# Kernel tuning notes

Hardware: AMD Instinct MI355X
Metric: run time of the kernel (lower is better)

Reference implementation:

```python
import jax, jax.numpy as jnp
import numpy as np

LAMBDA = 10.0
BETA = 10.0
W = 5  # window size per axis (5,5,5); padding=2 hardcoded in original
DN = ('NCDHW', 'OIDHW', 'NCDHW')


def box_mean(x):
    """Uniform 5x5x5 box-filter mean with zero padding=2, via separable 1D convs."""
    specs = [((1, 1, W, 1, 1), [(2, 2), (0, 0), (0, 0)]),
             ((1, 1, 1, W, 1), [(0, 0), (2, 2), (0, 0)]),
             ((1, 1, 1, 1, W), [(0, 0), (0, 0), (2, 2)])]
    for kshape, pads in specs:
        k = jnp.full(kshape, 1.0 / W, dtype=x.dtype)
        x = jax.lax.conv_general_dilated(x, k, (1, 1, 1), pads, dimension_numbers=DN)
    return x


def lcc_loss(gt, pred):
    omega = gt.size
    d_gt = gt - box_mean(gt)
    d_pred = pred - box_mean(pred)
    num = jnp.square(jnp.sum(d_gt * d_pred))
    den = jnp.sum(jnp.square(d_gt)) * jnp.sum(jnp.square(d_pred))
    den = jnp.maximum(den, 1e-5)
    return -(1.0 / omega) * (num / den)


def reg_field_loss(reg_gt, reg_pred):
    omega = reg_gt.size
    return jnp.sqrt(jnp.sum(jnp.square(reg_pred - reg_gt))) / omega


def tversky_loss2(seg_gt, seg_pred):
    den = jnp.maximum(jnp.sum(seg_gt + seg_pred), 1e-5)
    return -0.5 * jnp.sum(2.0 * seg_gt * seg_pred) / den


def setup_inputs() -> dict:
    key = jax.random.key(0)
    ks = jax.random.split(key, 10)
    shp_f = (2, 3, 128, 128, 128)
    shp_i = (2, 1, 128, 128, 128)
    return {
        'F_0': jax.random.normal(ks[0], shp_f, jnp.float32),
        'F_0g': jax.random.normal(ks[1], shp_f, jnp.float32),
        'I_0': jax.random.uniform(ks[2], shp_i, jnp.float32),
        'I_0R': jax.random.uniform(ks[3], shp_i, jnp.float32),
        'I_1': jax.random.uniform(ks[4], shp_i, jnp.float32),
        'I_1R': jax.random.uniform(ks[5], shp_i, jnp.float32),
        'S_0': jax.random.uniform(ks[6], shp_i, jnp.float32),
        'S_0g': jax.random.uniform(ks[7], shp_i, jnp.float32),
        'S_1': jax.random.uniform(ks[8], shp_i, jnp.float32),
        'S_1g': jax.random.uniform(ks[9], shp_i, jnp.float32),
    }


def reference(F_0, F_0g, I_0, I_0R, I_1, I_1R, S_0, S_0g, S_1, S_1g):
    return (reg_field_loss(F_0, F_0g)
            + LAMBDA * (lcc_loss(I_0, I_0R) + lcc_loss(I_1, I_1R))
            + BETA * (tversky_loss2(S_0, S_0g) + tversky_loss2(S_1, S_1g)))
```

## Files before the change

### kernel.cpp

```cpp
#include <hip/hip_runtime.h>
#include <math.h>

#define VOL   (128*128*128)
#define PLANE (128*128)

#define LCC_BLOCKS   1024
#define SQ_BLOCKS    1024
#define TV_BLOCKS    256
#define TOTAL_BLOCKS (LCC_BLOCKS + SQ_BLOCKS + 2 * TV_BLOCKS)


__device__ __forceinline__ double wave_reduce_d(double v) {
    #pragma unroll
    for (int off = 32; off > 0; off >>= 1)
        v += __shfl_down(v, off, 64);
    return v;
}

__device__ __forceinline__ void block_reduce1_atomic(double a, double* dst) {
    __shared__ double s1[4];
    int lane = threadIdx.x & 63;
    int wave = threadIdx.x >> 6;
    a = wave_reduce_d(a);
    if (lane == 0) s1[wave] = a;
    __syncthreads();
    if (threadIdx.x == 0) {
        double A = s1[0] + s1[1] + s1[2] + s1[3];
        atomicAdd(&dst[0], A);
    }
}

__device__ __forceinline__ void block_reduce2_atomic(double a, double b, double* dst) {
    __shared__ double s2[2][4];
    int lane = threadIdx.x & 63;
    int wave = threadIdx.x >> 6;
    a = wave_reduce_d(a);
    b = wave_reduce_d(b);
    if (lane == 0) { s2[0][wave] = a; s2[1][wave] = b; }
    __syncthreads();
    if (threadIdx.x == 0) {
        atomicAdd(&dst[0], s2[0][0] + s2[0][1] + s2[0][2] + s2[0][3]);
        atomicAdd(&dst[1], s2[1][0] + s2[1][1] + s2[1][2] + s2[1][3]);
    }
}

__device__ __forceinline__ void block_reduce3_atomic(double a, double b, double c, double* dst) {
    __shared__ double s3[3][4];
    int lane = threadIdx.x & 63;
    int wave = threadIdx.x >> 6;
    a = wave_reduce_d(a);
    b = wave_reduce_d(b);
    c = wave_reduce_d(c);
    if (lane == 0) { s3[0][wave] = a; s3[1][wave] = b; s3[2][wave] = c; }
    __syncthreads();
    if (threadIdx.x == 0) {
        atomicAdd(&dst[0], s3[0][0] + s3[0][1] + s3[0][2] + s3[0][3]);
        atomicAdd(&dst[1], s3[1][0] + s3[1][1] + s3[1][2] + s3[1][3]);
        atomicAdd(&dst[2], s3[2][0] + s3[2][1] + s3[2][2] + s3[2][3]);
    }
}


__global__ void zero_ws_kernel(double* ws) {
    if (threadIdx.x < 16) ws[threadIdx.x] = 0.0;
}


__global__ __launch_bounds__(256) void mega_kernel(
    const float* __restrict__ F0,  const float* __restrict__ F0g,
    const float* __restrict__ I0,  const float* __restrict__ I0R,
    const float* __restrict__ I1,  const float* __restrict__ I1R,
    const float* __restrict__ S0,  const float* __restrict__ S0g,
    const float* __restrict__ S1,  const float* __restrict__ S1g,
    double* __restrict__ ws)
{
    int b = blockIdx.x;
    int tid = threadIdx.x;

    if (b < LCC_BLOCKS) {
        __shared__ float ybuf[2 * 8 * 128];
        __shared__ float dbuf[8 * 128];

        int pair = b >> 9;
        int r  = b & 511;
        int y0 = (r & 15) << 3;
        int z0 = ((r >> 4) & 15) << 3;
        int n  = r >> 8;

        const float* gt = pair ? I1  : I0;
        const float* pr = pair ? I1R : I0R;
        double* dst = ws + (pair ? 4 : 1);

        int x = tid & 127;
        int g = tid >> 7;
        const float* V = (g ? pr : gt) + (size_t)n * VOL;

        float a1 = 0.f, a2 = 0.f, a3 = 0.f;
        float ps[5][8];
        float cent1[8], cent2[8];
        float v[12];

        float* yb = ybuf + g * 1024;

        {
            int zp = z0 - 2;
            bool zin = (zp >= 0);
            #pragma unroll
            for (int j = 0; j < 12; ++j) {
                int gy = y0 - 2 + j;
                v[j] = (zin && gy >= 0 && gy < 128)
                         ? V[(size_t)zp * PLANE + (size_t)gy * 128 + x] : 0.0f;
            }
        }

        #pragma unroll
        for (int it = 0; it < 12; ++it) {
            int zp = z0 - 2 + it;
            #pragma unroll
            for (int k = 0; k < 8; ++k)
                yb[k * 128 + x] = v[k] + v[k+1] + v[k+2] + v[k+3] + v[k+4];

            float vn[12];
            if (it < 11) {
                int zq = zp + 1;
                bool zin = (zq < 128);
                bool zlo = (zq >= 0);
                #pragma unroll
                for (int j = 0; j < 12; ++j) {
                    int gy = y0 - 2 + j;
                    vn[j] = (zin && zlo && gy >= 0 && gy < 128)
                              ? V[(size_t)zq * PLANE + (size_t)gy * 128 + x] : 0.0f;
                }
            }
            __syncthreads();

            #pragma unroll
            for (int k = 0; k < 8; ++k) {
                float s = yb[k * 128 + x];
                if (x >= 2)   s += yb[k * 128 + x - 2];
                if (x >= 1)   s += yb[k * 128 + x - 1];
                if (x <= 126) s += yb[k * 128 + x + 1];
                if (x <= 125) s += yb[k * 128 + x + 2];
                ps[it % 5][k] = s;
            }

            float d[8];
            if (it >= 4) {
                #pragma unroll
                for (int k = 0; k < 8; ++k) {
                    float m = (ps[0][k] + ps[1][k] + ps[2][k] + ps[3][k] + ps[4][k])
                              * (1.0f / 125.0f);
                    d[k] = cent2[k] - m;
                }
                if (g) {
                    #pragma unroll
                    for (int k = 0; k < 8; ++k) {
                        dbuf[k * 128 + x] = d[k];
                        a3 += d[k] * d[k];
                    }
                }
            }
            __syncthreads();
            if (it >= 4 && g == 0) {
                #pragma unroll
                for (int k = 0; k < 8; ++k) {
                    float dp = dbuf[k * 128 + x];
                    a1 += d[k] * dp;
                    a2 += d[k] * d[k];
                }
            }

            #pragma unroll
            for (int k = 0; k < 8; ++k) { cent2[k] = cent1[k]; cent1[k] = v[k + 2]; }
            if (it < 11) {
                #pragma unroll
                for (int j = 0; j < 12; ++j) v[j] = vn[j];
            }
        }
        block_reduce3_atomic((double)a1, (double)a2, (double)a3, dst);

    } else if (b < LCC_BLOCKS + SQ_BLOCKS) {
        int bid = b - LCC_BLOCKS;
        const float4* A = (const float4*)F0;
        const float4* B = (const float4*)F0g;
        int n4 = 12582912 / 4;
        int idx = bid * 256 + tid;
        int stride = SQ_BLOCKS * 256;
        float acc = 0.f;
        for (int i = idx; i < n4; i += stride) {
            float4 xx = A[i], yy = B[i];
            float d0 = yy.x - xx.x, d1 = yy.y - xx.y;
            float d2 = yy.z - xx.z, d3 = yy.w - xx.w;
            acc += (d0 * d0 + d1 * d1) + (d2 * d2 + d3 * d3);
        }
        block_reduce1_atomic((double)acc, &ws[0]);

    } else {
        int bid = b - (LCC_BLOCKS + SQ_BLOCKS);
        int pair = bid >= TV_BLOCKS;
        bid -= pair ? TV_BLOCKS : 0;
        const float4* Gp = (const float4*)(pair ? S1 : S0);
        const float4* Pp = (const float4*)(pair ? S1g : S0g);
        double* dst = ws + (pair ? 9 : 7);
        int n4 = 4194304 / 4;
        int idx = bid * 256 + tid;
        int stride = TV_BLOCKS * 256;
        float asum = 0.f, aprod = 0.f;
        for (int i = idx; i < n4; i += stride) {
            float4 xx = Gp[i], yy = Pp[i];
            asum  += (xx.x + yy.x) + (xx.y + yy.y) + (xx.z + yy.z) + (xx.w + yy.w);
            aprod += (xx.x * yy.x + xx.y * yy.y) + (xx.z * yy.z + xx.w * yy.w);
        }
        block_reduce2_atomic((double)asum, (double)aprod, dst);
    }
}

__global__ void finalize_kernel(const double* __restrict__ ws, float* out) {
    if (threadIdx.x == 0 && blockIdx.x == 0) {
        double reg = sqrt(ws[0]) / 12582912.0;

        double num0 = ws[1] * ws[1];
        double den0 = ws[2] * ws[3];
        if (den0 < 1e-5) den0 = 1e-5;
        double l0 = -(1.0 / 4194304.0) * (num0 / den0);

        double num1 = ws[4] * ws[4];
        double den1 = ws[5] * ws[6];
        if (den1 < 1e-5) den1 = 1e-5;
        double l1 = -(1.0 / 4194304.0) * (num1 / den1);

        double td0 = ws[7]; if (td0 < 1e-5) td0 = 1e-5;
        double t0 = -ws[8] / td0;
        double td1 = ws[9]; if (td1 < 1e-5) td1 = 1e-5;
        double t1 = -ws[10] / td1;

        out[0] = (float)(reg + 10.0 * (l0 + l1) + 10.0 * (t0 + t1));
    }
}


extern "C" void kernel_launch(void* const* d_in, const int* in_sizes, int n_in,
                              void* d_out, int out_size, void* d_ws, size_t ws_size,
                              hipStream_t stream) {
    double* ws = (double*)d_ws;
    float* out = (float*)d_out;

    const float* F0  = (const float*)d_in[0];
    const float* F0g = (const float*)d_in[1];
    const float* I0  = (const float*)d_in[2];
    const float* I0R = (const float*)d_in[3];
    const float* I1  = (const float*)d_in[4];
    const float* I1R = (const float*)d_in[5];
    const float* S0  = (const float*)d_in[6];
    const float* S0g = (const float*)d_in[7];
    const float* S1  = (const float*)d_in[8];
    const float* S1g = (const float*)d_in[9];

    zero_ws_kernel<<<1, 64, 0, stream>>>(ws);
    mega_kernel<<<TOTAL_BLOCKS, 256, 0, stream>>>(F0, F0g, I0, I0R, I1, I1R,
                                                  S0, S0g, S1, S1g, ws);
    finalize_kernel<<<1, 64, 0, stream>>>(ws, out);
}
```

Measured before the change: 260.6 us.

## Restructure LCC box filter into per-wave tiles and interleave block roles

```diff
diff --git a/kernel.cpp b/kernel.cpp
--- a/kernel.cpp
+++ b/kernel.cpp
@@ -4,10 +4,10 @@
 #define VOL   (128*128*128)
 #define PLANE (128*128)
 
-#define LCC_BLOCKS   1024
+#define LCC_BLOCKS   512
 #define SQ_BLOCKS    1024
-#define TV_BLOCKS    256
-#define TOTAL_BLOCKS (LCC_BLOCKS + SQ_BLOCKS + 2 * TV_BLOCKS)
+#define TV_BLOCKS    512
+#define TOTAL_BLOCKS 2048
 
 
 __device__ __forceinline__ double wave_reduce_d(double v) {
@@ -24,10 +24,8 @@
     a = wave_reduce_d(a);
     if (lane == 0) s1[wave] = a;
     __syncthreads();
-    if (threadIdx.x == 0) {
-        double A = s1[0] + s1[1] + s1[2] + s1[3];
-        atomicAdd(&dst[0], A);
-    }
+    if (threadIdx.x == 0)
+        atomicAdd(&dst[0], s1[0] + s1[1] + s1[2] + s1[3]);
 }
 
 __device__ __forceinline__ void block_reduce2_atomic(double a, double b, double* dst) {
@@ -76,118 +74,117 @@
 {
     int b = blockIdx.x;
     int tid = threadIdx.x;
-
-    if (b < LCC_BLOCKS) {
-        __shared__ float ybuf[2 * 8 * 128];
-        __shared__ float dbuf[8 * 128];
-
-        int pair = b >> 9;
-        int r  = b & 511;
-        int y0 = (r & 15) << 3;
-        int z0 = ((r >> 4) & 15) << 3;
-        int n  = r >> 8;
-
-        const float* gt = pair ? I1  : I0;
-        const float* pr = pair ? I1R : I0R;
+    int r = b & 3;
+
+    if (r == 0) {
+        __shared__ float xrow[4][2][4][68];
+
+        int lb = b >> 2;
+        int w  = tid >> 6;
+        int l  = tid & 63;
+        int wid = lb * 4 + w;
+        int pair  = wid >> 10;
+        int batch = (wid >> 9) & 1;
+        int zs    = (wid >> 6) & 7;
+        int yt    = (wid >> 1) & 31;
+        int xt    = wid & 1;
+        int x0 = xt << 6, y0 = yt << 2, z0 = zs << 4;
+
+        const float* Vg = (pair ? I1  : I0)  + (size_t)batch * VOL;
+        const float* Vp = (pair ? I1R : I0R) + (size_t)batch * VOL;
         double* dst = ws + (pair ? 4 : 1);
 
-        int x = tid & 127;
-        int g = tid >> 7;
-        const float* V = (g ? pr : gt) + (size_t)n * VOL;
-
+        int x  = x0 + l;
+        int hx = x0 + ((l < 2) ? (l - 2) : (62 + l));
+        int hxc = hx < 0 ? 0 : (hx > 127 ? 127 : hx);
+        bool hok = (hx >= 0) && (hx < 128);
+        int hslot = (l < 2) ? l : (64 + l);
+
+        float (*rowg)[68] = xrow[w][0];
+        float (*rowp)[68] = xrow[w][1];
+
+        float psg[5][4], psp[5][4];
+        float cg1[4] = {0,0,0,0}, cg2[4] = {0,0,0,0};
+        float cp1[4] = {0,0,0,0}, cp2[4] = {0,0,0,0};
         float a1 = 0.f, a2 = 0.f, a3 = 0.f;
-        float ps[5][8];
-        float cent1[8], cent2[8];
-        float v[12];
-
-        float* yb = ybuf + g * 1024;
-
-        {
-            int zp = z0 - 2;
-            bool zin = (zp >= 0);
+
+        for (int o = 0; o < 4; ++o) {
             #pragma unroll
-            for (int j = 0; j < 12; ++j) {
-                int gy = y0 - 2 + j;
-                v[j] = (zin && gy >= 0 && gy < 128)
-                         ? V[(size_t)zp * PLANE + (size_t)gy * 128 + x] : 0.0f;
-            }
-        }
-
-        #pragma unroll
-        for (int it = 0; it < 12; ++it) {
-            int zp = z0 - 2 + it;
-            #pragma unroll
-            for (int k = 0; k < 8; ++k)
-                yb[k * 128 + x] = v[k] + v[k+1] + v[k+2] + v[k+3] + v[k+4];
-
-            float vn[12];
-            if (it < 11) {
-                int zq = zp + 1;
-                bool zin = (zq < 128);
-                bool zlo = (zq >= 0);
-                #pragma unroll
-                for (int j = 0; j < 12; ++j) {
+            for (int u = 0; u < 5; ++u) {
+                int it = o * 5 + u;
+                int zp = z0 - 2 + it;
+                bool zok = (zp >= 0) && (zp < 128);
+                int zpc = zp < 0 ? 0 : (zp > 127 ? 127 : zp);
+                size_t zoff = (size_t)zpc * PLANE;
+
+                float vg[8], vp[8], hg[8], hp[8];
+                #pragma unroll
+                for (int j = 0; j < 8; ++j) {
                     int gy = y0 - 2 + j;
-                    vn[j] = (zin && zlo && gy >= 0 && gy < 128)
-                              ? V[(size_t)zq * PLANE + (size_t)gy * 128 + x] : 0.0f;
-                }
-            }
-            __syncthreads();
-
-            #pragma unroll
-            for (int k = 0; k < 8; ++k) {
-                float s = yb[k * 128 + x];
-                if (x >= 2)   s += yb[k * 128 + x - 2];
-                if (x >= 1)   s += yb[k * 128 + x - 1];
-                if (x <= 126) s += yb[k * 128 + x + 1];
-                if (x <= 125) s += yb[k * 128 + x + 2];
-                ps[it % 5][k] = s;
-            }
-
-            float d[8];
-            if (it >= 4) {
-                #pragma unroll
-                for (int k = 0; k < 8; ++k) {
-                    float m = (ps[0][k] + ps[1][k] + ps[2][k] + ps[3][k] + ps[4][k])
-                              * (1.0f / 125.0f);
-                    d[k] = cent2[k] - m;
-                }
-                if (g) {
+                    bool ok = zok && (gy >= 0) && (gy < 128);
+                    int gyc = gy < 0 ? 0 : (gy > 127 ? 127 : gy);
+                    size_t ro = zoff + (size_t)gyc * 128;
+                    float tg = Vg[ro + x];
+                    float tp = Vp[ro + x];
+                    vg[j] = ok ? tg : 0.0f;
+                    vp[j] = ok ? tp : 0.0f;
+                    float thg = 0.0f, thp = 0.0f;
+                    if (l < 4) { thg = Vg[ro + hxc]; thp = Vp[ro + hxc]; }
+                    hg[j] = (ok && hok) ? thg : 0.0f;
+                    hp[j] = (ok && hok) ? thp : 0.0f;
+                }
+                #pragma unroll
+                for (int k = 0; k < 4; ++k) {
+                    rowg[k][2 + l] = vg[k] + vg[k+1] + vg[k+2] + vg[k+3] + vg[k+4];
+                    rowp[k][2 + l] = vp[k] + vp[k+1] + vp[k+2] + vp[k+3] + vp[k+4];
+                }
+                if (l < 4) {
                     #pragma unroll
-                    for (int k = 0; k < 8; ++k) {
-                        dbuf[k * 128 + x] = d[k];
-                        a3 += d[k] * d[k];
+                    for (int k = 0; k < 4; ++k) {
+                        rowg[k][hslot] = hg[k] + hg[k+1] + hg[k+2] + hg[k+3] + hg[k+4];
+                        rowp[k][hslot] = hp[k] + hp[k+1] + hp[k+2] + hp[k+3] + hp[k+4];
                     }
                 }
-            }
-            __syncthreads();
-            if (it >= 4 && g == 0) {
-                #pragma unroll
-                for (int k = 0; k < 8; ++k) {
-                    float dp = dbuf[k * 128 + x];
-                    a1 += d[k] * dp;
-                    a2 += d[k] * d[k];
-                }
-            }
-
-            #pragma unroll
-            for (int k = 0; k < 8; ++k) { cent2[k] = cent1[k]; cent1[k] = v[k + 2]; }
-            if (it < 11) {
-                #pragma unroll
-                for (int j = 0; j < 12; ++j) v[j] = vn[j];
+                #pragma unroll
+                for (int k = 0; k < 4; ++k) {
+                    psg[u][k] = rowg[k][l] + rowg[k][l+1] + rowg[k][l+2]
+                              + rowg[k][l+3] + rowg[k][l+4];
+                    psp[u][k] = rowp[k][l] + rowp[k][l+1] + rowp[k][l+2]
+                              + rowp[k][l+3] + rowp[k][l+4];
+                }
+                if (it >= 4) {
+                    #pragma unroll
+                    for (int k = 0; k < 4; ++k) {
+                        float mg = (psg[0][k] + psg[1][k] + psg[2][k] + psg[3][k] + psg[4][k])
+                                   * (1.0f / 125.0f);
+                        float mp = (psp[0][k] + psp[1][k] + psp[2][k] + psp[3][k] + psp[4][k])
+                                   * (1.0f / 125.0f);
+                        float dg = cg2[k] - mg;
+                        float dp = cp2[k] - mp;
+                        a1 += dg * dp;
+                        a2 += dg * dg;
+                        a3 += dp * dp;
+                    }
+                }
+                #pragma unroll
+                for (int k = 0; k < 4; ++k) {
+                    cg2[k] = cg1[k]; cg1[k] = vg[k + 2];
+                    cp2[k] = cp1[k]; cp1[k] = vp[k + 2];
+                }
             }
         }
         block_reduce3_atomic((double)a1, (double)a2, (double)a3, dst);
 
-    } else if (b < LCC_BLOCKS + SQ_BLOCKS) {
-        int bid = b - LCC_BLOCKS;
+    } else if (r != 3) {
+        int bid = (b >> 2) * 2 + (r - 1);
         const float4* A = (const float4*)F0;
         const float4* B = (const float4*)F0g;
-        int n4 = 12582912 / 4;
         int idx = bid * 256 + tid;
-        int stride = SQ_BLOCKS * 256;
+        const int stride = SQ_BLOCKS * 256;
         float acc = 0.f;
-        for (int i = idx; i < n4; i += stride) {
+        #pragma unroll
+        for (int k = 0; k < 12; ++k) {
+            int i = idx + k * stride;
             float4 xx = A[i], yy = B[i];
             float d0 = yy.x - xx.x, d1 = yy.y - xx.y;
             float d2 = yy.z - xx.z, d3 = yy.w - xx.w;
@@ -196,17 +193,18 @@
         block_reduce1_atomic((double)acc, &ws[0]);
 
     } else {
-        int bid = b - (LCC_BLOCKS + SQ_BLOCKS);
-        int pair = bid >= TV_BLOCKS;
-        bid -= pair ? TV_BLOCKS : 0;
+        int idx0 = b >> 2;
+        int pair = idx0 >> 8;
+        int bid  = idx0 & 255;
         const float4* Gp = (const float4*)(pair ? S1 : S0);
         const float4* Pp = (const float4*)(pair ? S1g : S0g);
         double* dst = ws + (pair ? 9 : 7);
-        int n4 = 4194304 / 4;
         int idx = bid * 256 + tid;
-        int stride = TV_BLOCKS * 256;
+        const int stride = 256 * 256;
         float asum = 0.f, aprod = 0.f;
-        for (int i = idx; i < n4; i += stride) {
+        #pragma unroll
+        for (int k = 0; k < 16; ++k) {
+            int i = idx + k * stride;
             float4 xx = Gp[i], yy = Pp[i];
             asum  += (xx.x + yy.x) + (xx.y + yy.y) + (xx.z + yy.z) + (xx.w + yy.w);
             aprod += (xx.x * yy.x + xx.y * yy.y) + (xx.z * yy.z + xx.w * yy.w);
```

After: 312.5 us. 20.0% more time.
